# Kernel optimization log

Hardware: AMD Instinct MI355X
Metric: run time of the kernel (lower is better)

Reference implementation:

```python
import jax, jax.numpy as jnp
import numpy as np

N_MELS = 80
LSTM_DIM = 1024
ATT_DIM = 128
ENC_DIM = 512
PRENET = 256
LOC_FILT = 32
LOC_K = 31


def _lstm_step(x, h, c, k, r, b):
    z = x @ k + h @ r + b  # [B, 4*LSTM_DIM], keras gate order i,f,g,o
    i, f, g, o = jnp.split(z, 4, axis=-1)
    c2 = jax.nn.sigmoid(f) * c + jax.nn.sigmoid(i) * jnp.tanh(g)
    h2 = jax.nn.sigmoid(o) * jnp.tanh(c2)
    return h2, c2


def setup_inputs() -> dict:
    key = jax.random.key(0)
    ks = jax.random.split(key, 24)
    s = 0.05
    B, Tm, T = 32, 200, 400
    inp = {
        'memory': jax.random.normal(ks[0], (B, Tm, ENC_DIM), jnp.float32),
        'decoder_inputs': jax.random.normal(ks[1], (B, N_MELS, T), jnp.float32),
        # Prenet (2 dense+relu layers)
        'prenet_w0': jax.random.normal(ks[2], (N_MELS, PRENET)) * s,
        'prenet_b0': jnp.zeros((PRENET,)),
        'prenet_w1': jax.random.normal(ks[3], (PRENET, PRENET)) * s,
        'prenet_b1': jnp.zeros((PRENET,)),
        # LSTM 1: input = prenet(256) + context(512) = 768
        'lstm1_k': jax.random.normal(ks[4], (PRENET + ENC_DIM, 4 * LSTM_DIM)) * s,
        'lstm1_r': jax.random.normal(ks[5], (LSTM_DIM, 4 * LSTM_DIM)) * s,
        'lstm1_b': jnp.zeros((4 * LSTM_DIM,)),
        # LSTM 2: input = att_hidden(1024) + context(512) = 1536
        'lstm2_k': jax.random.normal(ks[6], (LSTM_DIM + ENC_DIM, 4 * LSTM_DIM)) * s,
        'lstm2_r': jax.random.normal(ks[7], (LSTM_DIM, 4 * LSTM_DIM)) * s,
        'lstm2_b': jnp.zeros((4 * LSTM_DIM,)),
        # Attention
        'wq': jax.random.normal(ks[8], (LSTM_DIM, ATT_DIM)) * s,
        'wm': jax.random.normal(ks[9], (ENC_DIM, ATT_DIM)) * s,
        'v': jax.random.normal(ks[10], (ATT_DIM,)) * s,
        'loc_conv': jax.random.normal(ks[11], (LOC_K, 2, LOC_FILT)) * s,  # WIO
        'loc_dense': jax.random.normal(ks[12], (LOC_FILT, ATT_DIM)) * s,
        # Projections: input = dec_hidden(1024) + context(512) = 1536
        'frame_w': jax.random.normal(ks[13], (LSTM_DIM + ENC_DIM, N_MELS)) * s,
        'frame_b': jnp.zeros((N_MELS,)),
        'stop_w': jax.random.normal(ks[14], (LSTM_DIM + ENC_DIM, 1)) * s,
        'stop_b': jnp.zeros((1,)),
    }
    return inp


def reference(memory, decoder_inputs, prenet_w0, prenet_b0, prenet_w1, prenet_b1,
              lstm1_k, lstm1_r, lstm1_b, lstm2_k, lstm2_r, lstm2_b,
              wq, wm, v, loc_conv, loc_dense, frame_w, frame_b, stop_w, stop_b):
    B, Tm, _ = memory.shape
    T = decoder_inputs.shape[2]

    # parse_decoder_inputs: [B, n_mels, T] -> [T, B, n_mels]; prepend go frame
    dec_in = jnp.transpose(decoder_inputs, (2, 0, 1))
    dec_in = jnp.concatenate([jnp.zeros((1, B, N_MELS), memory.dtype), dec_in], axis=0)
    # Prenet (dropout identity in inference mode)
    x = jax.nn.relu(dec_in @ prenet_w0 + prenet_b0)
    x = jax.nn.relu(x @ prenet_w1 + prenet_b1)  # [T+1, B, 256]

    processed_memory = jnp.tanh(memory @ wm)  # [B, Tm, ATT_DIM]

    def step(carry, xt):
        att_h, att_c, dec_h, dec_c, att_w, att_w_cum, att_ctx = carry
        # Attention RNN
        cell_in = jnp.concatenate([xt, att_ctx], axis=-1)
        att_h, att_c = _lstm_step(cell_in, att_h, att_c, lstm1_k, lstm1_r, lstm1_b)
        # Location-sensitive attention
        awc = jnp.stack([att_w, att_w_cum], axis=-1)  # [B, Tm, 2]
        loc = jax.lax.conv_general_dilated(awc, loc_conv, (1,), 'SAME',
                                           dimension_numbers=('NWC', 'WIO', 'NWC'))
        loc = jnp.tanh(loc @ loc_dense)  # [B, Tm, ATT_DIM]
        q = jnp.tanh(att_h @ wq)[:, None, :]  # [B, 1, ATT_DIM]
        energies = jnp.tanh(q + loc + processed_memory) @ v  # [B, Tm]
        att_w = jax.nn.softmax(energies, axis=1)
        att_ctx = jnp.einsum('bt,btd->bd', att_w, memory)  # [B, ENC_DIM]
        att_w_cum = att_w_cum + att_w
        # Decoder RNN
        dec_in2 = jnp.concatenate([att_h, att_ctx], axis=-1)
        dec_h, dec_c = _lstm_step(dec_in2, dec_h, dec_c, lstm2_k, lstm2_r, lstm2_b)
        dhac = jnp.concatenate([dec_h, att_ctx], axis=-1)
        mel = dhac @ frame_w + frame_b  # [B, n_mels]
        gate = jax.nn.sigmoid(dhac @ stop_w + stop_b)[:, 0]  # [B]
        carry = (att_h, att_c, dec_h, dec_c, att_w, att_w_cum, att_ctx)
        return carry, (mel, gate, att_w)

    z = jnp.zeros((B, LSTM_DIM), memory.dtype)
    zw = jnp.zeros((B, Tm), memory.dtype)
    zc = jnp.zeros((B, ENC_DIM), memory.dtype)
    carry0 = (z, z, z, z, zw, zw, zc)
    _, (mels, gates, aligns) = jax.lax.scan(step, carry0, x[:T])

    # parse_decoder_outputs
    mel_outputs = jnp.transpose(mels, (1, 2, 0))      # [B, n_mels, T]
    gate_outputs = jnp.transpose(gates, (1, 0))       # [B, T]
    alignments = jnp.transpose(aligns, (1, 0, 2))     # [B, T, Tm]
    return mel_outputs, gate_outputs, alignments
```

## Files before the change

### kernel.cpp

```cpp
#include <hip/hip_runtime.h>
#include <math.h>

#define TSTEPS 400

#define KSP1 7
#define KSP2 8

#define OFF_XPRE  0u
#define OFF_PM    1638400u
#define OFF_IN1T  2457600u
#define OFF_IN2T  2506752u
#define OFF_ZP1   2588672u
#define OFF_ZP2   3506176u
#define OFF_CTXP  4554752u
#define OFF_H2B   4620288u
#define OFF_C1    4685824u
#define OFF_C2    4718592u
#define OFF_ATTW  4751360u
#define OFF_CUM   4757760u
#define WS_FLOATS 4764160u

#define OUT_GATE  1024000
#define OUT_ALIGN 1036800

__device__ __forceinline__ float sigf(float x)   { return 1.f / (1.f + __expf(-x)); }
__device__ __forceinline__ float tanhf_(float x) { return 1.f - 2.f / (__expf(2.f*x) + 1.f); }

__global__ void __launch_bounds__(256) prenet_kernel(
    const float* __restrict__ dec, const float* __restrict__ w0, const float* __restrict__ b0,
    const float* __restrict__ w1, const float* __restrict__ b1, float* __restrict__ ws)
{
    __shared__ float s_in[80];
    __shared__ float s_h0[256];
    int t = blockIdx.x, b = blockIdx.y, tid = threadIdx.x;
    if (tid < 80) s_in[tid] = (t == 0) ? 0.f : dec[b*32000 + tid*400 + (t-1)];
    __syncthreads();
    float s = b0[tid];
    for (int m = 0; m < 80; ++m) s = fmaf(s_in[m], w0[m*256 + tid], s);
    s_h0[tid] = fmaxf(s, 0.f);
    __syncthreads();
    float s2 = b1[tid];
    for (int k = 0; k < 256; ++k) s2 = fmaf(s_h0[k], w1[k*256 + tid], s2);
    float v = fmaxf(s2, 0.f);
    unsigned u = __float_as_uint(v);
    u += 0x7fffu + ((u >> 16) & 1u);
    ((unsigned short*)(ws + OFF_XPRE))[(size_t)t*8192 + tid*32 + b] = (unsigned short)(u >> 16);
}

__global__ void __launch_bounds__(128) pmem_kernel(
    const float* __restrict__ mp, const float* __restrict__ wm, float* __restrict__ ws)
{
    int t = blockIdx.x, b = blockIdx.y, a = threadIdx.x;
    const float* mrow = mp + (b*200 + t)*512;
    float s = 0.f;
    for (int d = 0; d < 512; ++d) s = fmaf(mrow[d], wm[d*128 + a], s);
    ws[OFF_PM + (b*200 + t)*128 + a] = tanhf_(s);
}

__global__ void __launch_bounds__(256) zero_kernel(float* __restrict__ ws)
{
    int gid = blockIdx.x*256 + threadIdx.x, gsz = gridDim.x*256;
    for (int i = gid; i < 49152; i += gsz) ws[OFF_IN1T + i] = 0.f;
    for (int i = gid; i < 81920; i += gsz) ws[OFF_IN2T + i] = 0.f;
    for (int i = gid; i < 32768; i += gsz) { ws[OFF_C1 + i] = 0.f; ws[OFF_C2 + i] = 0.f; }
    for (int i = gid; i < 65536; i += gsz) { ws[OFF_CTXP + i] = 0.f; ws[OFF_H2B + i] = 0.f; }
    for (int i = gid; i < 6400;  i += gsz) { ws[OFF_ATTW + i] = 0.f; ws[OFF_CUM + i] = 0.f; }
}

#define FMA8(XA, XB, W)                                                                               \
    a[0].x = fmaf(XA.x, W.x, a[0].x); a[0].y = fmaf(XA.x, W.y, a[0].y); a[0].z = fmaf(XA.x, W.z, a[0].z); a[0].w = fmaf(XA.x, W.w, a[0].w); \
    a[1].x = fmaf(XA.y, W.x, a[1].x); a[1].y = fmaf(XA.y, W.y, a[1].y); a[1].z = fmaf(XA.y, W.z, a[1].z); a[1].w = fmaf(XA.y, W.w, a[1].w); \
    a[2].x = fmaf(XA.z, W.x, a[2].x); a[2].y = fmaf(XA.z, W.y, a[2].y); a[2].z = fmaf(XA.z, W.z, a[2].z); a[2].w = fmaf(XA.z, W.w, a[2].w); \
    a[3].x = fmaf(XA.w, W.x, a[3].x); a[3].y = fmaf(XA.w, W.y, a[3].y); a[3].z = fmaf(XA.w, W.z, a[3].z); a[3].w = fmaf(XA.w, W.w, a[3].w); \
    a[4].x = fmaf(XB.x, W.x, a[4].x); a[4].y = fmaf(XB.x, W.y, a[4].y); a[4].z = fmaf(XB.x, W.z, a[4].z); a[4].w = fmaf(XB.x, W.w, a[4].w); \
    a[5].x = fmaf(XB.y, W.x, a[5].x); a[5].y = fmaf(XB.y, W.y, a[5].y); a[5].z = fmaf(XB.y, W.z, a[5].z); a[5].w = fmaf(XB.y, W.w, a[5].w); \
    a[6].x = fmaf(XB.z, W.x, a[6].x); a[6].y = fmaf(XB.z, W.y, a[6].y); a[6].z = fmaf(XB.z, W.z, a[6].z); a[6].w = fmaf(XB.z, W.w, a[6].w); \
    a[7].x = fmaf(XB.w, W.x, a[7].x); a[7].y = fmaf(XB.w, W.y, a[7].y); a[7].z = fmaf(XB.w, W.z, a[7].z); a[7].w = fmaf(XB.w, W.w, a[7].w)

__global__ void __launch_bounds__(512, 4) kernel_P1(
    const float* __restrict__ l1k, const float* __restrict__ l1r,
    const float* __restrict__ l2k, const float* __restrict__ l2r,
    float* __restrict__ ws, int t)
{
    __shared__ float s_acc[12288];
    const int tid = threadIdx.x, bid = blockIdx.x;
    const int jq = tid & 31, bgrp = (tid >> 5) & 3, ksub = tid >> 7;
    const int b0 = bgrp*8;
    float4 a[8];
#pragma unroll
    for (int i = 0; i < 8; ++i) a[i] = make_float4(0.f, 0.f, 0.f, 0.f);

    if (bid < 224) {
        if (t >= TSTEPS) return;
        const int colgrp = bid & 31, ksp = bid >> 5;
        const int j = colgrp*128 + jq*4;
        const float* in1m = ws + OFF_IN1T - 8192;
        const int k0 = ksp*256 + ksub*64;
        if (ksp == 0) {
            const unsigned short* xp = (const unsigned short*)(ws + OFF_XPRE) + (size_t)t*8192;
#pragma unroll 2
            for (int k = k0; k < k0 + 64; ++k) {
                float4 w = *(const float4*)(l1k + (size_t)k*4096 + j);
                uint4 xr = *(const uint4*)(xp + k*32 + b0);
                const unsigned short* xs = (const unsigned short*)&xr;
#pragma unroll
                for (int i = 0; i < 8; ++i) {
                    float x = __uint_as_float(((unsigned)xs[i]) << 16);
                    a[i].x = fmaf(x, w.x, a[i].x); a[i].y = fmaf(x, w.y, a[i].y);
                    a[i].z = fmaf(x, w.z, a[i].z); a[i].w = fmaf(x, w.w, a[i].w);
                }
            }
        } else {
            const int k0e = k0 + 64;
            if (k0 < 768) {
#pragma unroll 2
                for (int k = k0; k < k0e; ++k) {
                    float4 w = *(const float4*)(l1k + (size_t)k*4096 + j);
                    float4 xa = *(const float4*)(in1m + k*32 + b0);
                    float4 xb = *(const float4*)(in1m + k*32 + b0 + 4);
                    FMA8(xa, xb, w);
                }
            } else {
#pragma unroll 2
                for (int k = k0; k < k0e; ++k) {
                    float4 w = *(const float4*)(l1r + (size_t)(k - 768)*4096 + j);
                    float4 xa = *(const float4*)(in1m + k*32 + b0);
                    float4 xb = *(const float4*)(in1m + k*32 + b0 + 4);
                    FMA8(xa, xb, w);
                }
            }
        }
        if (ksub) {
#pragma unroll
            for (int i = 0; i < 8; ++i)
                *(float4*)(s_acc + (ksub-1)*4096 + (b0 + i)*128 + jq*4) = a[i];
        }
        __syncthreads();
        if (!ksub) {
            float* zp1 = ws + OFF_ZP1;
#pragma unroll
            for (int i = 0; i < 8; ++i) {
                float4 r0 = *(const float4*)(s_acc +          (b0 + i)*128 + jq*4);
                float4 r1 = *(const float4*)(s_acc +  4096 + (b0 + i)*128 + jq*4);
                float4 r2 = *(const float4*)(s_acc +  8192 + (b0 + i)*128 + jq*4);
                a[i].x += r0.x + r1.x + r2.x; a[i].y += r0.y + r1.y + r2.y;
                a[i].z += r0.z + r1.z + r2.z; a[i].w += r0.w + r1.w + r2.w;
                *(float4*)(zp1 + (size_t)(ksp*32 + b0 + i)*4096 + j) = a[i];
            }
        }
    } else {
        if (t < 1 || t > TSTEPS) return;
        const int g = bid - 224;
        const int colgrp = g & 31, ksp = g >> 5;
        const int j = colgrp*128 + jq*4;
        const float* in2T = ws + OFF_IN2T;
        const int k0 = ksp*320 + ksub*80;
        const int kend = k0 + 80;
        const int ka = min(kend, 1536);
#pragma unroll 2
        for (int k = k0; k < ka; ++k) {
            float4 w = *(const float4*)(l2k + (size_t)k*4096 + j);
            float4 xa = *(const float4*)(in2T + k*32 + b0);
            float4 xb = *(const float4*)(in2T + k*32 + b0 + 4);
            FMA8(xa, xb, w);
        }
        const int kb = max(k0, 1536);
#pragma unroll 2
        for (int k = kb; k < kend; ++k) {
            float4 w = *(const float4*)(l2r + (size_t)(k - 1536)*4096 + j);
            float4 xa = *(const float4*)(in2T + k*32 + b0);
            float4 xb = *(const float4*)(in2T + k*32 + b0 + 4);
            FMA8(xa, xb, w);
        }
        if (ksub) {
#pragma unroll
            for (int i = 0; i < 8; ++i)
                *(float4*)(s_acc + (ksub-1)*4096 + (b0 + i)*128 + jq*4) = a[i];
        }
        __syncthreads();
        if (!ksub) {
            float* zp2 = ws + OFF_ZP2;
#pragma unroll
            for (int i = 0; i < 8; ++i) {
                float4 r0 = *(const float4*)(s_acc +          (b0 + i)*128 + jq*4);
                float4 r1 = *(const float4*)(s_acc +  4096 + (b0 + i)*128 + jq*4);
                float4 r2 = *(const float4*)(s_acc +  8192 + (b0 + i)*128 + jq*4);
                a[i].x += r0.x + r1.x + r2.x; a[i].y += r0.y + r1.y + r2.y;
                a[i].z += r0.z + r1.z + r2.z; a[i].w += r0.w + r1.w + r2.w;
                *(float4*)(zp2 + (size_t)(ksp*32 + b0 + i)*4096 + j) = a[i];
            }
        }
    }
}

__global__ void __launch_bounds__(1024) kernel_P2(
    const float* __restrict__ mp, const float* __restrict__ l1b, const float* __restrict__ l2b,
    const float* __restrict__ wq, const float* __restrict__ vvec,
    const float* __restrict__ lconv, const float* __restrict__ ldense,
    const float* __restrict__ fw, const float* __restrict__ fb,
    const float* __restrict__ sw, const float* __restrict__ sb,
    float* __restrict__ ws, float* __restrict__ out, int t)
{
    __shared__ float s_attw[200], s_cum[200];
    __shared__ float s_hid[1024], s_q[128], s_ex[200], s_den[1];
    __shared__ float s_co[200*33];
    __shared__ float s_red[1024];
    const int tid = threadIdx.x, bid = blockIdx.x;
    float* in1m = ws + OFF_IN1T - 8192;
    float* in2T = ws + OFF_IN2T;
    float* zp1  = ws + OFF_ZP1;
    float* zp2  = ws + OFF_ZP2;
    float* ctxp = ws + OFF_CTXP;
    float* h2bb = ws + OFF_H2B;
    float* c1a  = ws + OFF_C1;
    float* c2a  = ws + OFF_C2;
    float* attw = ws + OFF_ATTW;
    float* cum  = ws + OFF_CUM;
    const float* pm = ws + OFF_PM;

    if (bid < 32) {
        if (t >= TSTEPS) return;
        const int b = bid;
        {
            int u = tid;
            float zi = l1b[u], zf = l1b[1024+u], zg = l1b[2048+u], zo = l1b[3072+u];
#pragma unroll
            for (int kc = 0; kc < KSP1; ++kc) {
                const float* zr = zp1 + (size_t)(kc*32 + b)*4096;
                zi += zr[u]; zf += zr[1024+u]; zg += zr[2048+u]; zo += zr[3072+u];
            }
            float c = sigf(zf)*c1a[b*1024+u] + sigf(zi)*tanhf_(zg);
            float h = sigf(zo)*tanhf_(c);
            c1a[b*1024+u] = c;
            s_hid[u] = h;
            in1m[(768+u)*32 + b] = h;
            in2T[u*32 + b] = h;
        }
        if (tid < 200) { s_attw[tid] = attw[b*200 + tid]; s_cum[tid] = cum[b*200 + tid]; }
        __syncthreads();
        {
            int a = tid & 127, kq = tid >> 7;
            float s = 0.f;
            for (int k = kq*128; k < kq*128 + 128; ++k)
                s = fmaf(s_hid[k], wq[k*128 + a], s);
            s_red[tid] = s;
        }
        __syncthreads();
        if (tid < 128) {
            float s = 0.f;
#pragma unroll
            for (int q = 0; q < 8; ++q) s += s_red[q*128 + tid];
            s_q[tid] = tanhf_(s);
        }
        for (int idx = tid; idx < 6400; idx += 1024) {
            int tl = idx >> 5, f = idx & 31;
            float s = 0.f;
            for (int dw = 0; dw < 31; ++dw) {
                int tg = tl - 15 + dw;
                if (tg >= 0 && tg < 200) {
                    s = fmaf(s_attw[tg], lconv[(dw*2+0)*32 + f], s);
                    s = fmaf(s_cum[tg],  lconv[(dw*2+1)*32 + f], s);
                }
            }
            s_co[tl*33 + f] = s;
        }
        __syncthreads();
        if (tid < 800) {
            int tl = tid >> 2, aq = tid & 3;
            const float* pmrow = pm + (b*200 + tl)*128;
            float e = 0.f;
            for (int a = aq*32; a < aq*32 + 32; ++a) {
                float s = 0.f;
#pragma unroll
                for (int f = 0; f < 32; ++f) s = fmaf(s_co[tl*33 + f], ldense[f*128 + a], s);
                float en = tanhf_(s_q[a] + tanhf_(s) + pmrow[a]);
                e = fmaf(en, vvec[a], e);
            }
            e += __shfl_xor(e, 1, 4);
            e += __shfl_xor(e, 2, 4);
            if (aq == 0) s_ex[tl] = __expf(e);
        }
        __syncthreads();
        if (tid < 64) {
            float s = 0.f;
            for (int i = tid; i < 200; i += 64) s += s_ex[i];
            for (int off = 32; off; off >>= 1) s += __shfl_down(s, off, 64);
            if (tid == 0) s_den[0] = s;
        }
        __syncthreads();
        if (tid < 200) {
            float w = s_ex[tid] / s_den[0];
            s_attw[tid] = w;
            attw[b*200 + tid] = w;
            cum[b*200 + tid] = s_cum[tid] + w;
            out[OUT_ALIGN + (b*400 + t)*200 + tid] = w;
        }
        __syncthreads();
        {
            int d = tid & 511, th = tid >> 9;
            float s = 0.f;
            for (int tt = th*100; tt < th*100 + 100; ++tt)
                s = fmaf(s_attw[tt], mp[(b*200 + tt)*512 + d], s);
            s_red[tid] = s;
        }
        __syncthreads();
        if (tid < 512) {
            float cv = s_red[tid] + s_red[512 + tid];
            ctxp[(size_t)(t & 3)*16384 + b*512 + tid] = cv;
            in1m[(256 + tid)*32 + b] = cv;
            in2T[(1024 + tid)*32 + b] = cv;
        }
    } else if (bid < 64) {
        if (t < 1 || t > TSTEPS) return;
        const int b = bid - 32, t1 = t - 1;
        float* h2b = h2bb + (size_t)(t1 & 1)*32768;
        int u = tid;
        float zi = l2b[u], zf = l2b[1024+u], zg = l2b[2048+u], zo = l2b[3072+u];
#pragma unroll
        for (int kc = 0; kc < KSP2; ++kc) {
            const float* zr = zp2 + (size_t)(kc*32 + b)*4096;
            zi += zr[u]; zf += zr[1024+u]; zg += zr[2048+u]; zo += zr[3072+u];
        }
        float c = sigf(zf)*c2a[b*1024+u] + sigf(zi)*tanhf_(zg);
        float h = sigf(zo)*tanhf_(c);
        c2a[b*1024+u] = c;
        in2T[(1536+u)*32 + b] = h;
        h2b[u*32 + b] = h;
    } else if (bid < 74) {
        if (t < 2) return;
        const int t2 = t - 2;
        const int mc = bid - 64;
        const int m_l = tid & 7, b = (tid >> 3) & 31, kh = tid >> 8;
        const int m = mc*8 + m_l;
        const float* cp = ctxp + (size_t)((t2 & 3)*32 + b)*512;
        const float* h2b = h2bb + (size_t)(t2 & 1)*32768;
        float s = 0.f;
        for (int k = kh*384; k < kh*384 + 384; ++k) {
            float dv = (k < 1024) ? h2b[k*32 + b] : cp[k - 1024];
            s = fmaf(dv, fw[k*80 + m], s);
        }
        s_red[tid] = s;
        __syncthreads();
        if (tid < 256) {
            float v4 = s_red[tid] + s_red[256+tid] + s_red[512+tid] + s_red[768+tid];
            int b2 = tid >> 3, m2 = mc*8 + (tid & 7);
            out[(b2*80 + m2)*400 + t2] = v4 + fb[m2];
        }
    } else {
        if (t < 2) return;
        const int t2 = t - 2;
        const int b = tid >> 5, kh = tid & 31;
        const float* cp = ctxp + (size_t)((t2 & 3)*32 + b)*512;
        const float* h2b = h2bb + (size_t)(t2 & 1)*32768;
        float s = 0.f;
        for (int k = kh*48; k < kh*48 + 48; ++k) {
            float dv = (k < 1024) ? h2b[k*32 + b] : cp[k - 1024];
            s = fmaf(dv, sw[k], s);
        }
        s_red[b*32 + kh] = s;
        __syncthreads();
        if (tid < 32) {
            float z = 0.f;
#pragma unroll
            for (int i = 0; i < 32; ++i) z += s_red[tid*32 + i];
            out[OUT_GATE + tid*400 + t2] = sigf(z + sb[0]);
        }
    }
}

extern "C" void kernel_launch(void* const* d_in, const int* in_sizes, int n_in,
                              void* d_out, int out_size, void* d_ws, size_t ws_size,
                              hipStream_t stream) {
    (void)in_sizes; (void)n_in; (void)out_size;
    const float* mp    = (const float*)d_in[0];
    const float* dec   = (const float*)d_in[1];
    const float* pw0   = (const float*)d_in[2];
    const float* pb0   = (const float*)d_in[3];
    const float* pw1   = (const float*)d_in[4];
    const float* pb1   = (const float*)d_in[5];
    const float* l1k   = (const float*)d_in[6];
    const float* l1r   = (const float*)d_in[7];
    const float* l1b   = (const float*)d_in[8];
    const float* l2k   = (const float*)d_in[9];
    const float* l2r   = (const float*)d_in[10];
    const float* l2b   = (const float*)d_in[11];
    const float* wq    = (const float*)d_in[12];
    const float* wm    = (const float*)d_in[13];
    const float* vvec  = (const float*)d_in[14];
    const float* lconv = (const float*)d_in[15];
    const float* ldns  = (const float*)d_in[16];
    const float* fw    = (const float*)d_in[17];
    const float* fb    = (const float*)d_in[18];
    const float* sw    = (const float*)d_in[19];
    const float* sb    = (const float*)d_in[20];
    float* ws  = (float*)d_ws;
    float* out = (float*)d_out;

    if (ws_size < (size_t)WS_FLOATS * sizeof(float)) return;

    prenet_kernel<<<dim3(400, 32), 256, 0, stream>>>(dec, pw0, pb0, pw1, pb1, ws);
    pmem_kernel  <<<dim3(200, 32), 128, 0, stream>>>(mp, wm, ws);
    zero_kernel  <<<256, 256, 0, stream>>>(ws);

    for (int t = 0; t <= TSTEPS; ++t) {
        kernel_P1<<<480, 512, 0, stream>>>(l1k, l1r, l2k, l2r, ws, t);
        kernel_P2<<<75, 1024, 0, stream>>>(mp, l1b, l2b, wq, vvec, lconv, ldns,
                                           fw, fb, sw, sb, ws, out, t);
    }
    kernel_P2<<<75, 1024, 0, stream>>>(mp, l1b, l2b, wq, vvec, lconv, ldns,
                                       fw, fb, sw, sb, ws, out, TSTEPS + 1);
}
```

Measured before the change: 81.12 ms.

## Stage LSTM GEMV weights into LDS via async global_load_lds double buffering

The per-step LSTM gate matvec blocks now stream 32-row weight chunks into shared memory with the global_load_lds builtin, double-buffered so the next chunk loads while the current one is consumed. The block's input slice is also staged in shared memory. Each thread computes a 2-batch by 4-column tile over the full K-range of the block, which removes the split-K shared-memory reduction. Several loops in the attention and projection kernels also get unroll pragmas. The aim is to hide weight-load latency, at the cost of a barrier and a full vmcnt drain on every chunk.

Result: slower. 101.4 ms (+25.0%).

```diff
diff --git a/kernel.cpp b/kernel.cpp
--- a/kernel.cpp
+++ b/kernel.cpp
@@ -25,6 +25,11 @@
 
 __device__ __forceinline__ float sigf(float x)   { return 1.f / (1.f + __expf(-x)); }
 __device__ __forceinline__ float tanhf_(float x) { return 1.f - 2.f / (__expf(2.f*x) + 1.f); }
+
+__device__ __forceinline__ void gload_lds16(const float* g, float* l) {
+    __builtin_amdgcn_global_load_lds((const __attribute__((address_space(1))) void*)g,
+                                     (__attribute__((address_space(3))) void*)l, 16, 0, 0);
+}
 
 __global__ void __launch_bounds__(256) prenet_kernel(
     const float* __restrict__ dec, const float* __restrict__ w0, const float* __restrict__ b0,
@@ -67,129 +72,132 @@
     for (int i = gid; i < 6400;  i += gsz) { ws[OFF_ATTW + i] = 0.f; ws[OFF_CUM + i] = 0.f; }
 }
 
-#define FMA8(XA, XB, W)                                                                               \
-    a[0].x = fmaf(XA.x, W.x, a[0].x); a[0].y = fmaf(XA.x, W.y, a[0].y); a[0].z = fmaf(XA.x, W.z, a[0].z); a[0].w = fmaf(XA.x, W.w, a[0].w); \
-    a[1].x = fmaf(XA.y, W.x, a[1].x); a[1].y = fmaf(XA.y, W.y, a[1].y); a[1].z = fmaf(XA.y, W.z, a[1].z); a[1].w = fmaf(XA.y, W.w, a[1].w); \
-    a[2].x = fmaf(XA.z, W.x, a[2].x); a[2].y = fmaf(XA.z, W.y, a[2].y); a[2].z = fmaf(XA.z, W.z, a[2].z); a[2].w = fmaf(XA.z, W.w, a[2].w); \
-    a[3].x = fmaf(XA.w, W.x, a[3].x); a[3].y = fmaf(XA.w, W.y, a[3].y); a[3].z = fmaf(XA.w, W.z, a[3].z); a[3].w = fmaf(XA.w, W.w, a[3].w); \
-    a[4].x = fmaf(XB.x, W.x, a[4].x); a[4].y = fmaf(XB.x, W.y, a[4].y); a[4].z = fmaf(XB.x, W.z, a[4].z); a[4].w = fmaf(XB.x, W.w, a[4].w); \
-    a[5].x = fmaf(XB.y, W.x, a[5].x); a[5].y = fmaf(XB.y, W.y, a[5].y); a[5].z = fmaf(XB.y, W.z, a[5].z); a[5].w = fmaf(XB.y, W.w, a[5].w); \
-    a[6].x = fmaf(XB.z, W.x, a[6].x); a[6].y = fmaf(XB.z, W.y, a[6].y); a[6].z = fmaf(XB.z, W.z, a[6].z); a[6].w = fmaf(XB.z, W.w, a[6].w); \
-    a[7].x = fmaf(XB.w, W.x, a[7].x); a[7].y = fmaf(XB.w, W.y, a[7].y); a[7].z = fmaf(XB.w, W.z, a[7].z); a[7].w = fmaf(XB.w, W.w, a[7].w)
-
 __global__ void __launch_bounds__(512, 4) kernel_P1(
     const float* __restrict__ l1k, const float* __restrict__ l1r,
     const float* __restrict__ l2k, const float* __restrict__ l2r,
     float* __restrict__ ws, int t)
 {
-    __shared__ float s_acc[12288];
+    __shared__ float s_x[10240];
+    __shared__ float s_w[8192];
     const int tid = threadIdx.x, bid = blockIdx.x;
-    const int jq = tid & 31, bgrp = (tid >> 5) & 3, ksub = tid >> 7;
-    const int b0 = bgrp*8;
-    float4 a[8];
-#pragma unroll
-    for (int i = 0; i < 8; ++i) a[i] = make_float4(0.f, 0.f, 0.f, 0.f);
+    const int jq = tid & 31, bq = tid >> 5;
+    const int lane = tid & 63, wid = tid >> 6;
+    float4 a0 = make_float4(0.f,0.f,0.f,0.f), a1 = make_float4(0.f,0.f,0.f,0.f);
 
     if (bid < 224) {
         if (t >= TSTEPS) return;
         const int colgrp = bid & 31, ksp = bid >> 5;
         const int j = colgrp*128 + jq*4;
-        const float* in1m = ws + OFF_IN1T - 8192;
-        const int k0 = ksp*256 + ksub*64;
+        const float* wbase = (ksp < 3) ? (l1k + (size_t)ksp*256*4096)
+                                       : (l1r + (size_t)(ksp-3)*256*4096);
+        const float* gsrc = wbase + colgrp*128 + (lane & 31)*4 + (size_t)(lane >> 5)*4096
+                                  + (size_t)(wid*4)*4096;
+        float* ldst = s_w + wid*4*128;
+
+        {
+            const float* g = gsrc;
+            gload_lds16(g,            ldst);
+            gload_lds16(g + 2*4096,   ldst + 2*128);
+        }
         if (ksp == 0) {
-            const unsigned short* xp = (const unsigned short*)(ws + OFF_XPRE) + (size_t)t*8192;
-#pragma unroll 2
-            for (int k = k0; k < k0 + 64; ++k) {
-                float4 w = *(const float4*)(l1k + (size_t)k*4096 + j);
-                uint4 xr = *(const uint4*)(xp + k*32 + b0);
-                const unsigned short* xs = (const unsigned short*)&xr;
-#pragma unroll
-                for (int i = 0; i < 8; ++i) {
-                    float x = __uint_as_float(((unsigned)xs[i]) << 16);
-                    a[i].x = fmaf(x, w.x, a[i].x); a[i].y = fmaf(x, w.y, a[i].y);
-                    a[i].z = fmaf(x, w.z, a[i].z); a[i].w = fmaf(x, w.w, a[i].w);
-                }
+            const uint4* src = (const uint4*)((const unsigned short*)(ws + OFF_XPRE) + (size_t)t*8192);
+            for (int i = tid; i < 1024; i += 512) {
+                uint4 p = src[i];
+                float* d = s_x + i*8;
+                d[0] = __uint_as_float(p.x << 16); d[1] = __uint_as_float(p.x & 0xffff0000u);
+                d[2] = __uint_as_float(p.y << 16); d[3] = __uint_as_float(p.y & 0xffff0000u);
+                d[4] = __uint_as_float(p.z << 16); d[5] = __uint_as_float(p.z & 0xffff0000u);
+                d[6] = __uint_as_float(p.w << 16); d[7] = __uint_as_float(p.w & 0xffff0000u);
             }
         } else {
-            const int k0e = k0 + 64;
-            if (k0 < 768) {
-#pragma unroll 2
-                for (int k = k0; k < k0e; ++k) {
-                    float4 w = *(const float4*)(l1k + (size_t)k*4096 + j);
-                    float4 xa = *(const float4*)(in1m + k*32 + b0);
-                    float4 xb = *(const float4*)(in1m + k*32 + b0 + 4);
-                    FMA8(xa, xb, w);
-                }
-            } else {
-#pragma unroll 2
-                for (int k = k0; k < k0e; ++k) {
-                    float4 w = *(const float4*)(l1r + (size_t)(k - 768)*4096 + j);
-                    float4 xa = *(const float4*)(in1m + k*32 + b0);
-                    float4 xb = *(const float4*)(in1m + k*32 + b0 + 4);
-                    FMA8(xa, xb, w);
-                }
-            }
-        }
-        if (ksub) {
-#pragma unroll
-            for (int i = 0; i < 8; ++i)
-                *(float4*)(s_acc + (ksub-1)*4096 + (b0 + i)*128 + jq*4) = a[i];
-        }
-        __syncthreads();
-        if (!ksub) {
-            float* zp1 = ws + OFF_ZP1;
-#pragma unroll
-            for (int i = 0; i < 8; ++i) {
-                float4 r0 = *(const float4*)(s_acc +          (b0 + i)*128 + jq*4);
-                float4 r1 = *(const float4*)(s_acc +  4096 + (b0 + i)*128 + jq*4);
-                float4 r2 = *(const float4*)(s_acc +  8192 + (b0 + i)*128 + jq*4);
-                a[i].x += r0.x + r1.x + r2.x; a[i].y += r0.y + r1.y + r2.y;
-                a[i].z += r0.z + r1.z + r2.z; a[i].w += r0.w + r1.w + r2.w;
-                *(float4*)(zp1 + (size_t)(ksp*32 + b0 + i)*4096 + j) = a[i];
-            }
-        }
+            const float4* src = (const float4*)(ws + OFF_IN1T - 8192 + (size_t)ksp*256*32);
+            float4* dst = (float4*)s_x;
+            for (int i = tid; i < 2048; i += 512) dst[i] = src[i];
+        }
+        asm volatile("s_waitcnt vmcnt(0)" ::: "memory");
+        __syncthreads();
+
+        const float* xb = s_x + bq*2;
+        const float* wjb = s_w + jq*4;
+        for (int c = 0; c < 8; ++c) {
+            if (c + 1 < 8) {
+                const float* g = gsrc + (size_t)(c + 1)*32*4096;
+                float* lp = ldst + ((c + 1) & 1)*4096;
+                gload_lds16(g,          lp);
+                gload_lds16(g + 2*4096, lp + 2*128);
+            }
+            const float* wch = wjb + (c & 1)*4096;
+            const float* xch = xb + c*32*32;
+#pragma unroll 8
+            for (int kk = 0; kk < 32; ++kk) {
+                float4 w = *(const float4*)(wch + kk*128);
+                float2 x = *(const float2*)(xch + kk*32);
+                a0.x = fmaf(x.x, w.x, a0.x); a0.y = fmaf(x.x, w.y, a0.y);
+                a0.z = fmaf(x.x, w.z, a0.z); a0.w = fmaf(x.x, w.w, a0.w);
+                a1.x = fmaf(x.y, w.x, a1.x); a1.y = fmaf(x.y, w.y, a1.y);
+                a1.z = fmaf(x.y, w.z, a1.z); a1.w = fmaf(x.y, w.w, a1.w);
+            }
+            asm volatile("s_waitcnt vmcnt(0)" ::: "memory");
+            __syncthreads();
+        }
+        float* zp1 = ws + OFF_ZP1;
+        *(float4*)(zp1 + (size_t)(ksp*32 + bq*2 + 0)*4096 + j) = a0;
+        *(float4*)(zp1 + (size_t)(ksp*32 + bq*2 + 1)*4096 + j) = a1;
     } else {
         if (t < 1 || t > TSTEPS) return;
-        const int g = bid - 224;
-        const int colgrp = g & 31, ksp = g >> 5;
+        const int g2 = bid - 224;
+        const int colgrp = g2 & 31, ksp = g2 >> 5;
         const int j = colgrp*128 + jq*4;
-        const float* in2T = ws + OFF_IN2T;
-        const int k0 = ksp*320 + ksub*80;
-        const int kend = k0 + 80;
-        const int ka = min(kend, 1536);
-#pragma unroll 2
-        for (int k = k0; k < ka; ++k) {
-            float4 w = *(const float4*)(l2k + (size_t)k*4096 + j);
-            float4 xa = *(const float4*)(in2T + k*32 + b0);
-            float4 xb = *(const float4*)(in2T + k*32 + b0 + 4);
-            FMA8(xa, xb, w);
-        }
-        const int kb = max(k0, 1536);
-#pragma unroll 2
-        for (int k = kb; k < kend; ++k) {
-            float4 w = *(const float4*)(l2r + (size_t)(k - 1536)*4096 + j);
-            float4 xa = *(const float4*)(in2T + k*32 + b0);
-            float4 xb = *(const float4*)(in2T + k*32 + b0 + 4);
-            FMA8(xa, xb, w);
-        }
-        if (ksub) {
-#pragma unroll
-            for (int i = 0; i < 8; ++i)
-                *(float4*)(s_acc + (ksub-1)*4096 + (b0 + i)*128 + jq*4) = a[i];
-        }
-        __syncthreads();
-        if (!ksub) {
-            float* zp2 = ws + OFF_ZP2;
-#pragma unroll
-            for (int i = 0; i < 8; ++i) {
-                float4 r0 = *(const float4*)(s_acc +          (b0 + i)*128 + jq*4);
-                float4 r1 = *(const float4*)(s_acc +  4096 + (b0 + i)*128 + jq*4);
-                float4 r2 = *(const float4*)(s_acc +  8192 + (b0 + i)*128 + jq*4);
-                a[i].x += r0.x + r1.x + r2.x; a[i].y += r0.y + r1.y + r2.y;
-                a[i].z += r0.z + r1.z + r2.z; a[i].w += r0.w + r1.w + r2.w;
-                *(float4*)(zp2 + (size_t)(ksp*32 + b0 + i)*4096 + j) = a[i];
-            }
-        }
+        const int kbase = ksp*320;
+        float* ldst = s_w + wid*4*128;
+
+        {
+            int kg = kbase;
+            const float* wb2 = (kg < 1536) ? (l2k + (size_t)kg*4096)
+                                           : (l2r + (size_t)(kg - 1536)*4096);
+            const float* g = wb2 + colgrp*128 + (lane & 31)*4 + (size_t)(lane >> 5)*4096
+                                 + (size_t)(wid*4)*4096;
+            gload_lds16(g,          ldst);
+            gload_lds16(g + 2*4096, ldst + 2*128);
+        }
+        {
+            const float4* src = (const float4*)(ws + OFF_IN2T + (size_t)kbase*32);
+            float4* dst = (float4*)s_x;
+            for (int i = tid; i < 2560; i += 512) dst[i] = src[i];
+        }
+        asm volatile("s_waitcnt vmcnt(0)" ::: "memory");
+        __syncthreads();
+
+        const float* xb = s_x + bq*2;
+        const float* wjb = s_w + jq*4;
+        for (int c = 0; c < 10; ++c) {
+            if (c + 1 < 10) {
+                int kg = kbase + (c + 1)*32;
+                const float* wb2 = (kg < 1536) ? (l2k + (size_t)kg*4096)
+                                               : (l2r + (size_t)(kg - 1536)*4096);
+                const float* g = wb2 + colgrp*128 + (lane & 31)*4 + (size_t)(lane >> 5)*4096
+                                     + (size_t)(wid*4)*4096;
+                float* lp = ldst + ((c + 1) & 1)*4096;
+                gload_lds16(g,          lp);
+                gload_lds16(g + 2*4096, lp + 2*128);
+            }
+            const float* wch = wjb + (c & 1)*4096;
+            const float* xch = xb + c*32*32;
+#pragma unroll 8
+            for (int kk = 0; kk < 32; ++kk) {
+                float4 w = *(const float4*)(wch + kk*128);
+                float2 x = *(const float2*)(xch + kk*32);
+                a0.x = fmaf(x.x, w.x, a0.x); a0.y = fmaf(x.x, w.y, a0.y);
+                a0.z = fmaf(x.x, w.z, a0.z); a0.w = fmaf(x.x, w.w, a0.w);
+                a1.x = fmaf(x.y, w.x, a1.x); a1.y = fmaf(x.y, w.y, a1.y);
+                a1.z = fmaf(x.y, w.z, a1.z); a1.w = fmaf(x.y, w.w, a1.w);
+            }
+            asm volatile("s_waitcnt vmcnt(0)" ::: "memory");
+            __syncthreads();
+        }
+        float* zp2 = ws + OFF_ZP2;
+        *(float4*)(zp2 + (size_t)(ksp*32 + bq*2 + 0)*4096 + j) = a0;
+        *(float4*)(zp2 + (size_t)(ksp*32 + bq*2 + 1)*4096 + j) = a1;
     }
 }
 
@@ -241,6 +249,7 @@
         {
             int a = tid & 127, kq = tid >> 7;
             float s = 0.f;
+#pragma unroll 8
             for (int k = kq*128; k < kq*128 + 128; ++k)
                 s = fmaf(s_hid[k], wq[k*128 + a], s);
             s_red[tid] = s;
@@ -269,6 +278,7 @@
             int tl = tid >> 2, aq = tid & 3;
             const float* pmrow = pm + (b*200 + tl)*128;
             float e = 0.f;
+#pragma unroll 2
             for (int a = aq*32; a < aq*32 + 32; ++a) {
                 float s = 0.f;
 #pragma unroll
@@ -299,6 +309,7 @@
         {
             int d = tid & 511, th = tid >> 9;
             float s = 0.f;
+#pragma unroll 10
             for (int tt = th*100; tt < th*100 + 100; ++tt)
                 s = fmaf(s_attw[tt], mp[(b*200 + tt)*512 + d], s);
             s_red[tid] = s;
@@ -335,6 +346,7 @@
         const float* cp = ctxp + (size_t)((t2 & 3)*32 + b)*512;
         const float* h2b = h2bb + (size_t)(t2 & 1)*32768;
         float s = 0.f;
+#pragma unroll 8
         for (int k = kh*384; k < kh*384 + 384; ++k) {
             float dv = (k < 1024) ? h2b[k*32 + b] : cp[k - 1024];
             s = fmaf(dv, fw[k*80 + m], s);
@@ -353,6 +365,7 @@
         const float* cp = ctxp + (size_t)((t2 & 3)*32 + b)*512;
         const float* h2b = h2bb + (size_t)(t2 & 1)*32768;
         float s = 0.f;
+#pragma unroll 8
         for (int k = kh*48; k < kh*48 + 48; ++k) {
             float dv = (k < 1024) ? h2b[k*32 + b] : cp[k - 1024];
             s = fmaf(dv, sw[k], s);
```
